# Kernel tuning notes

Measured on AMD Instinct MI355X. Metric: run time of the kernel, lower is better.

Reference implementation:

```python
import jax, jax.numpy as jnp
import numpy as np

DEPTH = 2; C = 96; DIN = 192; R = 6; N = 16; K = 4
B = 1; H0 = 64; W0 = 64; L0 = H0 * W0


def layer_norm(x, g, b, eps=1e-5):
    m = jnp.mean(x, -1, keepdims=True)
    v = jnp.var(x, -1, keepdims=True)
    return (x - m) / jnp.sqrt(v + eps) * g + b


def selective_scan(u, delta, A, Bs, Cs, D):
    # u, delta: (B, KD, L); A: (KD, N); Bs, Cs: (B, K, N, L); D: (KD,)
    Bb, KD, L = u.shape
    Kk = Bs.shape[1]; Dd = KD // Kk; Nn = A.shape[1]
    dA = jnp.exp(delta[..., None] * A[None, :, None, :])              # (B,KD,L,N)
    Bfull = jnp.broadcast_to(Bs[:, :, None], (Bb, Kk, Dd, Nn, L)).reshape(Bb, KD, Nn, L)
    Cfull = jnp.broadcast_to(Cs[:, :, None], (Bb, Kk, Dd, Nn, L)).reshape(Bb, KD, Nn, L)
    dBu = delta[..., None] * Bfull.transpose(0, 1, 3, 2) * u[..., None]  # (B,KD,L,N)
    Ct = Cfull.transpose(3, 0, 1, 2)                                   # (L,B,KD,N)

    def step(h, inp):
        dA_t, dBu_t, C_t = inp
        h = dA_t * h + dBu_t
        return h, jnp.sum(h * C_t, -1)

    init = jnp.zeros((Bb, KD, Nn), u.dtype)
    _, ys = jax.lax.scan(step, init, (dA.transpose(2, 0, 1, 3), dBu.transpose(2, 0, 1, 3), Ct))
    y = ys.transpose(1, 2, 0)                                          # (B,KD,L)
    return y + D[None, :, None] * u


def ss2d(x, in_proj_w, conv_w, conv_b, x_proj_w, dt_w, dt_b, A_logs, Ds, outn_g, outn_b, out_proj_w):
    # x: (B,H,W,C)
    Bb, H, W, Cc = x.shape
    L = H * W
    xz = x @ in_proj_w.T                                  # (B,H,W,2*DIN)
    Din = xz.shape[-1] // 2
    xc, z = xz[..., :Din], xz[..., Din:]
    xc = xc.transpose(0, 3, 1, 2)                         # (B,DIN,H,W)
    xc = jax.lax.conv_general_dilated(xc, conv_w, (1, 1), 'SAME',
                                      feature_group_count=Din,
                                      dimension_numbers=('NCHW', 'OIHW', 'NCHW'))
    xc = jax.nn.silu(xc + conv_b[None, :, None, None])
    # cross-scan: 4 directions
    x0 = xc.reshape(Bb, Din, L)
    x1 = xc.transpose(0, 1, 3, 2).reshape(Bb, Din, L)
    xs = jnp.stack([x0, x1, jnp.flip(x0, -1), jnp.flip(x1, -1)], 1)  # (B,K,DIN,L)
    x_dbl = jnp.einsum('bkdl,kcd->bkcl', xs, x_proj_w)
    dts, Bm, Cm = x_dbl[:, :, :R], x_dbl[:, :, R:R + N], x_dbl[:, :, R + N:]
    dts = jnp.einsum('bkrl,kdr->bkdl', dts, dt_w)
    u = xs.reshape(Bb, K * Din, L)
    delta = jax.nn.softplus(dts.reshape(Bb, K * Din, L) + dt_b.reshape(K * Din)[None, :, None])
    A = -jnp.exp(A_logs)                                  # (K*DIN, N)
    ys = selective_scan(u, delta, A, Bm, Cm, Ds).reshape(Bb, K, Din, L)
    # cross-merge
    y0 = ys[:, 0]
    y1 = ys[:, 1].reshape(Bb, Din, W, H).transpose(0, 1, 3, 2).reshape(Bb, Din, L)
    y2 = jnp.flip(ys[:, 2], -1)
    y3 = jnp.flip(ys[:, 3], -1).reshape(Bb, Din, W, H).transpose(0, 1, 3, 2).reshape(Bb, Din, L)
    y = (y0 + y1 + y2 + y3).transpose(0, 2, 1).reshape(Bb, H, W, Din)
    y = layer_norm(y, outn_g, outn_b)
    y = y * jax.nn.silu(z)
    return y @ out_proj_w.T                               # (B,H,W,C)


def setup_inputs() -> dict:
    key = jax.random.key(0)
    ks = jax.random.split(key, 10)
    f = jnp.float32
    rn = lambda k, s: jax.random.normal(k, s, f) * 0.02
    return {
        'x': jax.random.normal(ks[0], (B, L0, C), f),
        'H': H0, 'W': W0,
        'norm1_g': jnp.ones((DEPTH, C), f), 'norm1_b': jnp.zeros((DEPTH, C), f),
        'vssn_g': jnp.ones((DEPTH, C), f), 'vssn_b': jnp.zeros((DEPTH, C), f),
        'in_proj_w': rn(ks[1], (DEPTH, 2 * DIN, C)),
        'conv_w': rn(ks[2], (DEPTH, DIN, 1, 3, 3)),
        'conv_b': jnp.zeros((DEPTH, DIN), f),
        'x_proj_w': rn(ks[3], (DEPTH, K, R + 2 * N, DIN)),
        'dt_w': rn(ks[4], (DEPTH, K, DIN, R)),
        'dt_b': jax.random.uniform(ks[5], (DEPTH, K, DIN), f, -4.0, -2.0),
        'A_logs': jnp.log(jnp.broadcast_to(jnp.arange(1, N + 1, dtype=f), (DEPTH, K * DIN, N))),
        'Ds': jnp.ones((DEPTH, K * DIN), f),
        'outn_g': jnp.ones((DEPTH, DIN), f), 'outn_b': jnp.zeros((DEPTH, DIN), f),
        'out_proj_w': rn(ks[6], (DEPTH, C, DIN)),
        'res_conv_w': rn(ks[7], (C, C, 3, 3)),
        'res_conv_b': jnp.zeros((C,), f),
    }


def reference(x, H, W, norm1_g, norm1_b, vssn_g, vssn_b, in_proj_w, conv_w, conv_b,
              x_proj_w, dt_w, dt_b, A_logs, Ds, outn_g, outn_b, out_proj_w,
              res_conv_w, res_conv_b):
    Bb, Ll, Cc = x.shape
    shortcut = x
    for i in range(DEPTH):
        sc = x
        xn = layer_norm(x, norm1_g[i], norm1_b[i]).reshape(Bb, H, W, Cc)
        # VSSBlock: internal pre-norm + residual around SS2D (drop_path = 0)
        xi = xn + ss2d(layer_norm(xn, vssn_g[i], vssn_b[i]), in_proj_w[i], conv_w[i],
                       conv_b[i], x_proj_w[i], dt_w[i], dt_b[i], A_logs[i], Ds[i],
                       outn_g[i], outn_b[i], out_proj_w[i])
        x = sc + xi.reshape(Bb, Ll, Cc)
    xc = x.transpose(0, 2, 1).reshape(Bb, Cc, H, W)
    xc = jax.lax.conv_general_dilated(xc, res_conv_w, (1, 1), 'SAME',
                                      dimension_numbers=('NCHW', 'OIHW', 'NCHW'))
    xc = xc + res_conv_b[None, :, None, None]
    return xc.reshape(Bb, Cc, Ll).transpose(0, 2, 1) + shortcut
```

## Files before the change

### kernel.cpp

```cpp
#include <hip/hip_runtime.h>
#include <math.h>

#define LTOK 4096
#define CCH  96
#define DIN_ 192
#define KDIR 4
#define NST  16
#define KD_  768

#define O_XN     0
#define O_XZ     786432
#define O_XCONV  2359296
#define O_XCONVT 3145728
#define O_DELTA  3932160
#define O_BM     7077888
#define O_CM     7340032
#define O_YS     9961472
#define O_XCUR   13107200

__device__ __forceinline__ float siluf(float x) { return x / (1.f + __expf(-x)); }

__global__ void fusedA_kernel(const float* __restrict__ x, const float* __restrict__ g1,
                              const float* __restrict__ b1, const float* __restrict__ g2,
                              const float* __restrict__ b2, const float* __restrict__ w,
                              float* __restrict__ xn, float* __restrict__ xz) {
  __shared__ float As[96 * 72];
  __shared__ float Bs[96 * 68];
  int tid = threadIdx.x;
  int l0 = blockIdx.x * 64;
  int j0 = blockIdx.y * 64;
  int m = tid >> 2, j = tid & 3;
  int l = l0 + m;
  float v[24];
  float s = 0.f, ss = 0.f;
#pragma unroll
  for (int t = 0; t < 24; ++t) {
    int k = j + 4 * t;
    float vv = x[l * 96 + k];
    v[t] = vv; s += vv; ss += vv * vv;
  }
  s += __shfl_xor(s, 1); ss += __shfl_xor(ss, 1);
  s += __shfl_xor(s, 2); ss += __shfl_xor(ss, 2);
  float m1 = s * (1.f / 96.f);
  float rs1 = rsqrtf(ss * (1.f / 96.f) - m1 * m1 + 1e-5f);
  float s2 = 0.f, ss2 = 0.f;
#pragma unroll
  for (int t = 0; t < 24; ++t) {
    int k = j + 4 * t;
    float nv = (v[t] - m1) * rs1 * g1[k] + b1[k];
    v[t] = nv; s2 += nv; ss2 += nv * nv;
    if (blockIdx.y == 0) xn[l * 96 + k] = nv;
  }
  s2 += __shfl_xor(s2, 1); ss2 += __shfl_xor(ss2, 1);
  s2 += __shfl_xor(s2, 2); ss2 += __shfl_xor(ss2, 2);
  float m2 = s2 * (1.f / 96.f);
  float rs2 = rsqrtf(ss2 * (1.f / 96.f) - m2 * m2 + 1e-5f);
#pragma unroll
  for (int t = 0; t < 24; ++t) {
    int k = j + 4 * t;
    As[k * 72 + m] = (v[t] - m2) * rs2 * g2[k] + b2[k];
  }
  for (int qi = tid; qi < 64 * 24; qi += 256) {
    int nn = qi / 24, q = qi % 24;
    const float4 wv = *(const float4*)&w[(j0 + nn) * 96 + q * 4];
    Bs[(q * 4 + 0) * 68 + nn] = wv.x;
    Bs[(q * 4 + 1) * 68 + nn] = wv.y;
    Bs[(q * 4 + 2) * 68 + nn] = wv.z;
    Bs[(q * 4 + 3) * 68 + nn] = wv.w;
  }
  __syncthreads();
  int mg = tid & 15, ng = tid >> 4;
  float acc[4][4] = {};
  for (int k = 0; k < 96; ++k) {
    float a0 = As[k * 72 + 4 * mg + 0], a1 = As[k * 72 + 4 * mg + 1];
    float a2 = As[k * 72 + 4 * mg + 2], a3 = As[k * 72 + 4 * mg + 3];
    float b0 = Bs[k * 68 + 4 * ng + 0], b1_ = Bs[k * 68 + 4 * ng + 1];
    float b2_ = Bs[k * 68 + 4 * ng + 2], b3 = Bs[k * 68 + 4 * ng + 3];
    acc[0][0] += a0 * b0; acc[0][1] += a0 * b1_; acc[0][2] += a0 * b2_; acc[0][3] += a0 * b3;
    acc[1][0] += a1 * b0; acc[1][1] += a1 * b1_; acc[1][2] += a1 * b2_; acc[1][3] += a1 * b3;
    acc[2][0] += a2 * b0; acc[2][1] += a2 * b1_; acc[2][2] += a2 * b2_; acc[2][3] += a2 * b3;
    acc[3][0] += a3 * b0; acc[3][1] += a3 * b1_; acc[3][2] += a3 * b2_; acc[3][3] += a3 * b3;
  }
#pragma unroll
  for (int i = 0; i < 4; ++i) {
    float4 o = make_float4(acc[i][0], acc[i][1], acc[i][2], acc[i][3]);
    *(float4*)&xz[(l0 + 4 * mg + i) * 384 + j0 + 4 * ng] = o;
  }
}

__global__ void dwconvT_kernel(const float* __restrict__ xz, const float* __restrict__ cw,
                               const float* __restrict__ cb, float* __restrict__ xconv,
                               float* __restrict__ xconvT) {
  int w0 = blockIdx.x * 16, h0 = blockIdx.y * 16, d0 = blockIdx.z * 8;
  __shared__ float xs[324 * 9];
  int tid = threadIdx.x;
  for (int idx = tid; idx < 324 * 8; idx += 256) {
    int dd = idx & 7;
    int p = idx >> 3;
    int ph = p / 18, pw = p - ph * 18;
    int hh = h0 + ph - 1, ww = w0 + pw - 1;
    float v = 0.f;
    if (hh >= 0 && hh < 64 && ww >= 0 && ww < 64) v = xz[(hh * 64 + ww) * 384 + d0 + dd];
    xs[p * 9 + dd] = v;
  }
  __syncthreads();
  int wi = tid & 15, hi = tid >> 4;
  for (int dd = 0; dd < 8; ++dd) {
    int d = d0 + dd;
    float acc = cb[d];
    const float* wgt = cw + d * 9;
#pragma unroll
    for (int r = 0; r < 3; ++r)
#pragma unroll
      for (int c = 0; c < 3; ++c)
        acc += xs[((hi + r) * 18 + wi + c) * 9 + dd] * wgt[r * 3 + c];
    float o = siluf(acc);
    xconv[d * LTOK + (h0 + hi) * 64 + w0 + wi] = o;
    xconvT[d * LTOK + (w0 + wi) * 64 + h0 + hi] = o;
  }
}

__global__ __launch_bounds__(256) void projdelta_kernel(
    const float* __restrict__ xconv, const float* __restrict__ xconvT,
    const float* __restrict__ xpw, const float* __restrict__ dtw,
    const float* __restrict__ dtb, float* __restrict__ delta,
    float* __restrict__ Bm, float* __restrict__ Cm) {
  int chunk = blockIdx.x;
  int k = blockIdx.y;
  int l0 = chunk * 32;
  bool rev = (k >= 2);
  int lnat0 = rev ? (4064 - l0) : l0;
  const float* ub = ((k & 1) ? xconvT : xconv);
  __shared__ float Us[192 * 34];
  __shared__ float Ws[38 * 196];
  __shared__ float xdm[6 * 34];
  int tid = threadIdx.x;
  for (int idx = tid; idx < 192 * 8; idx += 256) {
    int q = idx & 7, d = idx >> 3;
    float4 v = *(const float4*)&ub[d * LTOK + lnat0 + 4 * q];
    *(float4*)&Us[d * 34 + 4 * q] = v;
  }
  for (int idx = tid; idx < 38 * 48; idx += 256) {
    int q = idx % 48, c = idx / 48;
    float4 v = *(const float4*)&xpw[(k * 38 + c) * 192 + 4 * q];
    *(float4*)&Ws[c * 196 + 4 * q] = v;
  }
  __syncthreads();
  int ip = tid & 31;
  int cg = tid >> 5;
  int crow[5];
#pragma unroll
  for (int j = 0; j < 5; ++j) {
    int c = cg * 5 + j;
    crow[j] = ((c < 38) ? c : 0) * 196;
  }
  float acc[5] = {};
  for (int d = 0; d < 192; d += 4) {
    float u0 = Us[(d + 0) * 34 + ip];
    float u1 = Us[(d + 1) * 34 + ip];
    float u2 = Us[(d + 2) * 34 + ip];
    float u3 = Us[(d + 3) * 34 + ip];
#pragma unroll
    for (int j = 0; j < 5; ++j) {
      const float4 wv = *(const float4*)&Ws[crow[j] + d];
      acc[j] += u0 * wv.x + u1 * wv.y + u2 * wv.z + u3 * wv.w;
    }
  }
  int i = rev ? (31 - ip) : ip;
  int l = l0 + i;
#pragma unroll
  for (int j = 0; j < 5; ++j) {
    int c = cg * 5 + j;
    if (c < 6)       xdm[c * 34 + ip] = acc[j];
    else if (c < 22) Bm[((k << 12) + l) * NST + (c - 6)] = acc[j];
    else if (c < 38) Cm[((k << 12) + l) * NST + (c - 22)] = acc[j];
  }
  __syncthreads();
  const float* dtwk = dtw + k * 192 * 6;
  const float* dtbk = dtb + k * 192;
  int dg = tid >> 5;
  for (int m = 0; m < 24; ++m) {
    int d = dg + 8 * m;
    float a = dtbk[d];
#pragma unroll
    for (int r = 0; r < 6; ++r) a += dtwk[d * 6 + r] * xdm[r * 34 + ip];
    float sp = (a > 20.f) ? a : log1pf(__expf(a));
    delta[(k * 192 + d) * LTOK + l] = sp;
  }
}

__global__ __launch_bounds__(512) void scan_fused(
    const float* __restrict__ delta, const float* __restrict__ Bm,
    const float* __restrict__ Cm, const float* __restrict__ xconv,
    const float* __restrict__ xconvT, const float* __restrict__ A_logs,
    const float* __restrict__ Ds, float* __restrict__ ys) {
  int kd = blockIdx.x;
  int k = kd / 192, d = kd - k * 192;
  int tid = threadIdx.x;
  int nq = tid & 7;
  int c = tid >> 3;
  const float* ub = ((k & 1) ? xconvT : xconv) + d * LTOK;
  bool rev = (k >= 2);
  float A0 = -__expf(A_logs[kd * 16 + 2 * nq + 0]);
  float A1 = -__expf(A_logs[kd * 16 + 2 * nq + 1]);
  const float* dp = delta + kd * LTOK;
  const float* bp = Bm + k * LTOK * NST;
  const float* cp = Cm + k * LTOK * NST;
  __shared__ float Ps[16 * 65], Qs[16 * 65], H0s[16 * 65];
  int l0 = c * 64;
  float h0 = 0.f, h1 = 0.f, P0 = 1.f, P1 = 1.f;
  for (int t = 0; t < 64; t += 4) {
    int l = l0 + t;
    float4 dlt4 = *(const float4*)(dp + l);
    float4 u4;
    if (!rev) u4 = *(const float4*)(ub + l);
    else { float4 tp = *(const float4*)(ub + 4092 - l); u4 = make_float4(tp.w, tp.z, tp.y, tp.x); }
#pragma unroll
    for (int s = 0; s < 4; ++s) {
      float dlt = (s == 0) ? dlt4.x : (s == 1) ? dlt4.y : (s == 2) ? dlt4.z : dlt4.w;
      float uu  = (s == 0) ? u4.x  : (s == 1) ? u4.y  : (s == 2) ? u4.z  : u4.w;
      float2 B2 = *(const float2*)(bp + (l + s) * NST + 2 * nq);
      float du = dlt * uu;
      float a0 = __expf(dlt * A0), a1 = __expf(dlt * A1);
      h0 = a0 * h0 + du * B2.x; h1 = a1 * h1 + du * B2.y;
      P0 *= a0; P1 *= a1;
    }
  }
  Ps[(2 * nq + 0) * 65 + c] = P0; Qs[(2 * nq + 0) * 65 + c] = h0;
  Ps[(2 * nq + 1) * 65 + c] = P1; Qs[(2 * nq + 1) * 65 + c] = h1;
  __syncthreads();
  {
    int wv = tid >> 6, lane = tid & 63;
#pragma unroll
    for (int r = 0; r < 2; ++r) {
      int nn = wv * 2 + r;
      float P = Ps[nn * 65 + lane];
      float S = Qs[nn * 65 + lane];
#pragma unroll
      for (int off = 1; off < 64; off <<= 1) {
        float pp = __shfl_up(P, off);
        float sp = __shfl_up(S, off);
        if (lane >= off) { S = sp * P + S; P = pp * P; }
      }
      float g0 = __shfl_up(S, 1);
      if (lane == 0) g0 = 0.f;
      H0s[nn * 65 + lane] = g0;
    }
  }
  __syncthreads();
  float Dv = Ds[kd];
  float* yk = ys + (k * DIN_ + d) * LTOK;
  h0 = H0s[(2 * nq + 0) * 65 + c];
  h1 = H0s[(2 * nq + 1) * 65 + c];
  for (int t = 0; t < 64; t += 4) {
    int l = l0 + t;
    float4 dlt4 = *(const float4*)(dp + l);
    float4 u4;
    if (!rev) u4 = *(const float4*)(ub + l);
    else { float4 tp = *(const float4*)(ub + 4092 - l); u4 = make_float4(tp.w, tp.z, tp.y, tp.x); }
    float y4[4];
#pragma unroll
    for (int s = 0; s < 4; ++s) {
      float dlt = (s == 0) ? dlt4.x : (s == 1) ? dlt4.y : (s == 2) ? dlt4.z : dlt4.w;
      float uu  = (s == 0) ? u4.x  : (s == 1) ? u4.y  : (s == 2) ? u4.z  : u4.w;
      float2 B2 = *(const float2*)(bp + (l + s) * NST + 2 * nq);
      float2 C2 = *(const float2*)(cp + (l + s) * NST + 2 * nq);
      float du = dlt * uu;
      float a0 = __expf(dlt * A0), a1 = __expf(dlt * A1);
      h0 = a0 * h0 + du * B2.x; h1 = a1 * h1 + du * B2.y;
      float p = h0 * C2.x + h1 * C2.y;
      p += __shfl_xor(p, 1);
      p += __shfl_xor(p, 2);
      p += __shfl_xor(p, 4);
      y4[s] = p + Dv * uu;
    }
    if (nq == 0) {
      if (k == 0) {
        *(float4*)(yk + l) = make_float4(y4[0], y4[1], y4[2], y4[3]);
      } else if (k == 2) {
        *(float4*)(yk + 4092 - l) = make_float4(y4[3], y4[2], y4[1], y4[0]);
      } else if (k == 1) {
#pragma unroll
        for (int s = 0; s < 4; ++s) yk[(t + s) * 64 + c] = y4[s];
      } else {
#pragma unroll
        for (int s = 0; s < 4; ++s) yk[(63 - (t + s)) * 64 + (63 - c)] = y4[s];
      }
    }
  }
}

__global__ void combine_out(const float* __restrict__ ys, const float* __restrict__ xz,
                            const float* __restrict__ xn, const float* __restrict__ xsrc,
                            const float* __restrict__ og, const float* __restrict__ ob,
                            const float* __restrict__ ow, float* __restrict__ xout) {
  __shared__ float Ys[192 * 33];
  __shared__ float Bs[64 * 100];
  int tid = threadIdx.x;
  int l0 = blockIdx.x * 32;
  for (int it = tid; it < 192 * 8; it += 256) {
    int d = it >> 3, g = it & 7;
    int l = l0 + g * 4;
    float4 a0 = *(const float4*)&ys[(0 * DIN_ + d) * LTOK + l];
    float4 a1 = *(const float4*)&ys[(1 * DIN_ + d) * LTOK + l];
    float4 a2 = *(const float4*)&ys[(2 * DIN_ + d) * LTOK + l];
    float4 a3 = *(const float4*)&ys[(3 * DIN_ + d) * LTOK + l];
    float* yr = &Ys[d * 33 + g * 4];
    yr[0] = a0.x + a1.x + a2.x + a3.x;
    yr[1] = a0.y + a1.y + a2.y + a3.y;
    yr[2] = a0.z + a1.z + a2.z + a3.z;
    yr[3] = a0.w + a1.w + a2.w + a3.w;
  }
  __syncthreads();
  {
    int m = tid >> 3, q = tid & 7;
    int l = l0 + m;
    float zval[24];
    const float* zp = xz + l * 384 + 192 + q * 24;
#pragma unroll
    for (int i = 0; i < 6; ++i) {
      float4 zv = *(const float4*)(zp + 4 * i);
      zval[4 * i + 0] = zv.x; zval[4 * i + 1] = zv.y;
      zval[4 * i + 2] = zv.z; zval[4 * i + 3] = zv.w;
    }
    float s = 0.f, ssum = 0.f;
    float vv[24];
#pragma unroll
    for (int i = 0; i < 24; ++i) {
      float v = Ys[(q * 24 + i) * 33 + m];
      vv[i] = v; s += v; ssum += v * v;
    }
    s += __shfl_xor(s, 1); ssum += __shfl_xor(ssum, 1);
    s += __shfl_xor(s, 2); ssum += __shfl_xor(ssum, 2);
    s += __shfl_xor(s, 4); ssum += __shfl_xor(ssum, 4);
    float mu = s * (1.f / 192.f);
    float rs = rsqrtf(ssum * (1.f / 192.f) - mu * mu + 1e-5f);
#pragma unroll
    for (int i = 0; i < 24; ++i) {
      int d = q * 24 + i;
      float yn = (vv[i] - mu) * rs * og[d] + ob[d];
      Ys[d * 33 + m] = yn * siluf(zval[i]);
    }
  }
  int mg = tid & 31, cg = tid >> 5;
  float acc[12] = {};
  for (int kc = 0; kc < 3; ++kc) {
    __syncthreads();
    for (int qi = tid; qi < 96 * 16; qi += 256) {
      int cix = qi / 16, q = qi % 16;
      const float4 wv = *(const float4*)&ow[cix * 192 + kc * 64 + q * 4];
      Bs[(q * 4 + 0) * 100 + cix] = wv.x;
      Bs[(q * 4 + 1) * 100 + cix] = wv.y;
      Bs[(q * 4 + 2) * 100 + cix] = wv.z;
      Bs[(q * 4 + 3) * 100 + cix] = wv.w;
    }
    __syncthreads();
    for (int kk = 0; kk < 64; ++kk) {
      float a = Ys[(kc * 64 + kk) * 33 + mg];
      const float* br = &Bs[kk * 100 + cg * 12];
#pragma unroll
      for (int jj = 0; jj < 12; ++jj) acc[jj] += a * br[jj];
    }
  }
  int ll = l0 + mg;
#pragma unroll
  for (int jj = 0; jj < 12; ++jj) {
    int cix = cg * 12 + jj;
    xout[ll * 96 + cix] = xsrc[ll * 96 + cix] + xn[ll * 96 + cix] + acc[jj];
  }
}

__global__ void resconv_part(const float* __restrict__ x, const float* __restrict__ w,
                             float* __restrict__ pbuf) {
  int tile = blockIdx.x;
  int cs = blockIdx.y;
  int th0 = (tile >> 3) * 8, tw0 = (tile & 7) * 8;
  int cbase = cs * 6;
  __shared__ float xs[600];
  __shared__ float wlds[96 * 6 * 12];
  int tid = threadIdx.x;
  for (int idx = tid; idx < 600; idx += 256) {
    int cc = idx % 6;
    int pos = idx / 6;
    int hh = th0 + pos / 10 - 1;
    int ww = tw0 + pos % 10 - 1;
    float v = 0.f;
    if (hh >= 0 && hh < 64 && ww >= 0 && ww < 64) v = x[(hh * 64 + ww) * 96 + cbase + cc];
    xs[cc * 100 + pos] = v;
  }
  for (int idx = tid; idx < 96 * 54; idx += 256) {
    int c0 = idx / 54, o = idx - c0 * 54;
    int cc = o / 9, t = o - cc * 9;
    wlds[(c0 * 6 + cc) * 12 + t] = w[c0 * 864 + (cbase + cc) * 9 + t];
  }
  __syncthreads();
  int lane = tid & 63;
  int th = lane >> 3, tw = lane & 7;
  int c0g = tid >> 6;
  float acc[24] = {};
  for (int cc = 0; cc < 6; ++cc) {
    float xv[9];
#pragma unroll
    for (int r = 0; r < 3; ++r)
#pragma unroll
      for (int q = 0; q < 3; ++q) xv[r * 3 + q] = xs[cc * 100 + (th + r) * 10 + tw + q];
#pragma unroll
    for (int j = 0; j < 24; ++j) {
      const float* wr = &wlds[((c0g * 24 + j) * 6 + cc) * 12];
      float4 w0 = *(const float4*)wr;
      float4 w1 = *(const float4*)(wr + 4);
      float w8 = wr[8];
      acc[j] += xv[0] * w0.x + xv[1] * w0.y + xv[2] * w0.z + xv[3] * w0.w
              + xv[4] * w1.x + xv[5] * w1.y + xv[6] * w1.z + xv[7] * w1.w + xv[8] * w8;
    }
  }
  int l = (th0 + th) * 64 + tw0 + tw;
  float* pb = pbuf + cs * 393216 + l * 96 + c0g * 24;
#pragma unroll
  for (int j = 0; j < 24; j += 4)
    *(float4*)(pb + j) = make_float4(acc[j], acc[j + 1], acc[j + 2], acc[j + 3]);
}

__global__ void resconv_reduce(const float* __restrict__ pbuf, const float* __restrict__ b,
                               const float* __restrict__ shortcut, float* __restrict__ out) {
  int i4 = blockIdx.x * 256 + threadIdx.x;
  int base = i4 * 4;
  int c4 = base % 96;
  float4 s = *(const float4*)(shortcut + base);
  float4 bb = *(const float4*)(b + c4);
  s.x += bb.x; s.y += bb.y; s.z += bb.z; s.w += bb.w;
#pragma unroll
  for (int ss = 0; ss < 16; ++ss) {
    float4 p = *(const float4*)(pbuf + ss * 393216 + base);
    s.x += p.x; s.y += p.y; s.z += p.z; s.w += p.w;
  }
  *(float4*)(out + base) = s;
}

extern "C" void kernel_launch(void* const* d_in, const int* in_sizes, int n_in,
                              void* d_out, int out_size, void* d_ws, size_t ws_size,
                              hipStream_t stream) {
  const float* x_in     = (const float*)d_in[0];
  const float* norm1_g  = (const float*)d_in[3];
  const float* norm1_b  = (const float*)d_in[4];
  const float* vssn_g   = (const float*)d_in[5];
  const float* vssn_b   = (const float*)d_in[6];
  const float* in_proj  = (const float*)d_in[7];
  const float* conv_w   = (const float*)d_in[8];
  const float* conv_b   = (const float*)d_in[9];
  const float* x_proj   = (const float*)d_in[10];
  const float* dt_w     = (const float*)d_in[11];
  const float* dt_b     = (const float*)d_in[12];
  const float* A_logs   = (const float*)d_in[13];
  const float* Ds       = (const float*)d_in[14];
  const float* outn_g   = (const float*)d_in[15];
  const float* outn_b   = (const float*)d_in[16];
  const float* out_proj = (const float*)d_in[17];
  const float* rc_w     = (const float*)d_in[18];
  const float* rc_b     = (const float*)d_in[19];

  float* ws = (float*)d_ws;
  float* xn    = ws + O_XN;
  float* xz    = ws + O_XZ;
  float* xconv = ws + O_XCONV;
  float* xconvT= ws + O_XCONVT;
  float* delta = ws + O_DELTA;
  float* Bm    = ws + O_BM;
  float* Cm    = ws + O_CM;
  float* ysb   = ws + O_YS;
  float* xcur  = ws + O_XCUR;
  float* pbuf  = ws + O_DELTA;

  const float* xsrc = x_in;
  for (int i = 0; i < 2; ++i) {
    fusedA_kernel<<<dim3(64, 6), 256, 0, stream>>>(xsrc,
        norm1_g + i * 96, norm1_b + i * 96, vssn_g + i * 96, vssn_b + i * 96,
        in_proj + i * 36864, xn, xz);
    dwconvT_kernel<<<dim3(4, 4, 24), 256, 0, stream>>>(xz, conv_w + i * 1728,
        conv_b + i * 192, xconv, xconvT);
    projdelta_kernel<<<dim3(128, 4), 256, 0, stream>>>(xconv, xconvT,
        x_proj + i * 29184, dt_w + i * 4608, dt_b + i * 768, delta, Bm, Cm);
    scan_fused<<<768, 512, 0, stream>>>(delta, Bm, Cm, xconv, xconvT,
        A_logs + i * 12288, Ds + i * 768, ysb);
    combine_out<<<128, 256, 0, stream>>>(ysb, xz, xn, xsrc,
        outn_g + i * 192, outn_b + i * 192, out_proj + i * 18432, xcur);
    xsrc = xcur;
  }
  resconv_part<<<dim3(64, 16), 256, 0, stream>>>(xcur, rc_w, pbuf);
  resconv_reduce<<<384, 256, 0, stream>>>(pbuf, rc_b, x_in, (float*)d_out);
}
```

Before: 381.0 us.

## Rebalance scan: 4 states per thread, 128 shorter chunks, two-stage prefix

The scan kernel now gives each thread 4 SSM states and 32-token chunks instead of 2 states and 64-token chunks, so each block has 128 chunks per state. The cross-chunk prefix combine becomes two 64-lane shuffle scans, with the second one seeded by the carry from the first. This shortens the serial recurrence per thread, uses wider float4 loads of B and C, and removes one shuffle stage in the output reduction. In exchange each thread holds more registers, the chunk-combine phase does more work, and the transposed output indexing had to be remapped.

```diff
diff --git a/kernel.cpp b/kernel.cpp
--- a/kernel.cpp
+++ b/kernel.cpp
@@ -197,19 +197,22 @@
   int kd = blockIdx.x;
   int k = kd / 192, d = kd - k * 192;
   int tid = threadIdx.x;
-  int nq = tid & 7;
-  int c = tid >> 3;
+  int nq = tid & 3;
+  int c = tid >> 2;
   const float* ub = ((k & 1) ? xconvT : xconv) + d * LTOK;
   bool rev = (k >= 2);
-  float A0 = -__expf(A_logs[kd * 16 + 2 * nq + 0]);
-  float A1 = -__expf(A_logs[kd * 16 + 2 * nq + 1]);
+  float A0 = -__expf(A_logs[kd * 16 + 4 * nq + 0]);
+  float A1 = -__expf(A_logs[kd * 16 + 4 * nq + 1]);
+  float A2 = -__expf(A_logs[kd * 16 + 4 * nq + 2]);
+  float A3 = -__expf(A_logs[kd * 16 + 4 * nq + 3]);
   const float* dp = delta + kd * LTOK;
   const float* bp = Bm + k * LTOK * NST;
   const float* cp = Cm + k * LTOK * NST;
-  __shared__ float Ps[16 * 65], Qs[16 * 65], H0s[16 * 65];
-  int l0 = c * 64;
-  float h0 = 0.f, h1 = 0.f, P0 = 1.f, P1 = 1.f;
-  for (int t = 0; t < 64; t += 4) {
+  __shared__ float Ps[16 * 132], Qs[16 * 132], H0s[16 * 132];
+  int l0 = c * 32;
+  float h0 = 0.f, h1 = 0.f, h2 = 0.f, h3 = 0.f;
+  float P0 = 1.f, P1 = 1.f, P2 = 1.f, P3 = 1.f;
+  for (int t = 0; t < 32; t += 4) {
     int l = l0 + t;
     float4 dlt4 = *(const float4*)(dp + l);
     float4 u4;
@@ -219,23 +222,27 @@
     for (int s = 0; s < 4; ++s) {
       float dlt = (s == 0) ? dlt4.x : (s == 1) ? dlt4.y : (s == 2) ? dlt4.z : dlt4.w;
       float uu  = (s == 0) ? u4.x  : (s == 1) ? u4.y  : (s == 2) ? u4.z  : u4.w;
-      float2 B2 = *(const float2*)(bp + (l + s) * NST + 2 * nq);
+      float4 B4 = *(const float4*)(bp + (l + s) * NST + 4 * nq);
       float du = dlt * uu;
       float a0 = __expf(dlt * A0), a1 = __expf(dlt * A1);
-      h0 = a0 * h0 + du * B2.x; h1 = a1 * h1 + du * B2.y;
-      P0 *= a0; P1 *= a1;
-    }
-  }
-  Ps[(2 * nq + 0) * 65 + c] = P0; Qs[(2 * nq + 0) * 65 + c] = h0;
-  Ps[(2 * nq + 1) * 65 + c] = P1; Qs[(2 * nq + 1) * 65 + c] = h1;
+      float a2 = __expf(dlt * A2), a3 = __expf(dlt * A3);
+      h0 = a0 * h0 + du * B4.x; h1 = a1 * h1 + du * B4.y;
+      h2 = a2 * h2 + du * B4.z; h3 = a3 * h3 + du * B4.w;
+      P0 *= a0; P1 *= a1; P2 *= a2; P3 *= a3;
+    }
+  }
+  Ps[(4 * nq + 0) * 132 + c] = P0; Qs[(4 * nq + 0) * 132 + c] = h0;
+  Ps[(4 * nq + 1) * 132 + c] = P1; Qs[(4 * nq + 1) * 132 + c] = h1;
+  Ps[(4 * nq + 2) * 132 + c] = P2; Qs[(4 * nq + 2) * 132 + c] = h2;
+  Ps[(4 * nq + 3) * 132 + c] = P3; Qs[(4 * nq + 3) * 132 + c] = h3;
   __syncthreads();
   {
     int wv = tid >> 6, lane = tid & 63;
 #pragma unroll
     for (int r = 0; r < 2; ++r) {
       int nn = wv * 2 + r;
-      float P = Ps[nn * 65 + lane];
-      float S = Qs[nn * 65 + lane];
+      float P = Ps[nn * 132 + lane];
+      float S = Qs[nn * 132 + lane];
 #pragma unroll
       for (int off = 1; off < 64; off <<= 1) {
         float pp = __shfl_up(P, off);
@@ -244,15 +251,32 @@
       }
       float g0 = __shfl_up(S, 1);
       if (lane == 0) g0 = 0.f;
-      H0s[nn * 65 + lane] = g0;
+      H0s[nn * 132 + lane] = g0;
+      float T0 = __shfl(S, 63);
+      float P1_ = Ps[nn * 132 + 64 + lane];
+      float S1_ = Qs[nn * 132 + 64 + lane];
+#pragma unroll
+      for (int off = 1; off < 64; off <<= 1) {
+        float pp = __shfl_up(P1_, off);
+        float sp = __shfl_up(S1_, off);
+        if (lane >= off) { S1_ = sp * P1_ + S1_; P1_ = pp * P1_; }
+      }
+      float gex = __shfl_up(S1_, 1);
+      float pex = __shfl_up(P1_, 1);
+      if (lane == 0) { gex = 0.f; pex = 1.f; }
+      H0s[nn * 132 + 64 + lane] = pex * T0 + gex;
     }
   }
   __syncthreads();
   float Dv = Ds[kd];
   float* yk = ys + (k * DIN_ + d) * LTOK;
-  h0 = H0s[(2 * nq + 0) * 65 + c];
-  h1 = H0s[(2 * nq + 1) * 65 + c];
-  for (int t = 0; t < 64; t += 4) {
+  h0 = H0s[(4 * nq + 0) * 132 + c];
+  h1 = H0s[(4 * nq + 1) * 132 + c];
+  h2 = H0s[(4 * nq + 2) * 132 + c];
+  h3 = H0s[(4 * nq + 3) * 132 + c];
+  int row1 = 32 * (c & 1);
+  int col1 = c >> 1;
+  for (int t = 0; t < 32; t += 4) {
     int l = l0 + t;
     float4 dlt4 = *(const float4*)(dp + l);
     float4 u4;
@@ -263,15 +287,16 @@
     for (int s = 0; s < 4; ++s) {
       float dlt = (s == 0) ? dlt4.x : (s == 1) ? dlt4.y : (s == 2) ? dlt4.z : dlt4.w;
       float uu  = (s == 0) ? u4.x  : (s == 1) ? u4.y  : (s == 2) ? u4.z  : u4.w;
-      float2 B2 = *(const float2*)(bp + (l + s) * NST + 2 * nq);
-      float2 C2 = *(const float2*)(cp + (l + s) * NST + 2 * nq);
+      float4 B4 = *(const float4*)(bp + (l + s) * NST + 4 * nq);
+      float4 C4 = *(const float4*)(cp + (l + s) * NST + 4 * nq);
       float du = dlt * uu;
       float a0 = __expf(dlt * A0), a1 = __expf(dlt * A1);
-      h0 = a0 * h0 + du * B2.x; h1 = a1 * h1 + du * B2.y;
-      float p = h0 * C2.x + h1 * C2.y;
+      float a2 = __expf(dlt * A2), a3 = __expf(dlt * A3);
+      h0 = a0 * h0 + du * B4.x; h1 = a1 * h1 + du * B4.y;
+      h2 = a2 * h2 + du * B4.z; h3 = a3 * h3 + du * B4.w;
+      float p = h0 * C4.x + h1 * C4.y + h2 * C4.z + h3 * C4.w;
       p += __shfl_xor(p, 1);
       p += __shfl_xor(p, 2);
-      p += __shfl_xor(p, 4);
       y4[s] = p + Dv * uu;
     }
     if (nq == 0) {
@@ -281,10 +306,10 @@
         *(float4*)(yk + 4092 - l) = make_float4(y4[3], y4[2], y4[1], y4[0]);
       } else if (k == 1) {
 #pragma unroll
-        for (int s = 0; s < 4; ++s) yk[(t + s) * 64 + c] = y4[s];
+        for (int s = 0; s < 4; ++s) yk[(row1 + t + s) * 64 + col1] = y4[s];
       } else {
 #pragma unroll
-        for (int s = 0; s < 4; ++s) yk[(63 - (t + s)) * 64 + (63 - c)] = y4[s];
+        for (int s = 0; s < 4; ++s) yk[(63 - row1 - (t + s)) * 64 + (63 - col1)] = y4[s];
       }
     }
   }
```

Result: faster. 355.9 us (median of 2 runs) (-6.6%).
